# Kernel tuning notes

Hardware: AMD Instinct MI355X
Metric: run time of the kernel (lower is better)

Reference implementation:

```python
import jax, jax.numpy as jnp
import numpy as np

BIT, RW, CW, YR, ID, ZC = 4, 8, 8, 512, 64, 512


def setup_inputs() -> dict:
    key = jax.random.key(0)
    ks = jax.random.split(key, 8)
    return {
        "X": jax.random.normal(ks[0], (4096, CW * ZC), dtype=jnp.float32),
        "Y": jax.random.uniform(ks[1], (BIT, RW, CW, YR, ID), dtype=jnp.float32),
        "Z": jax.random.uniform(ks[2], (BIT, RW, CW, ID, ZC), dtype=jnp.float32),
        "a": jax.random.normal(ks[3], (BIT, RW, CW, 1, 1), dtype=jnp.float32),
        "b": jax.random.normal(ks[4], (BIT, RW, CW, 1, 1), dtype=jnp.float32),
        "c": jax.random.normal(ks[5], (BIT, RW, CW, 1, 1), dtype=jnp.float32),
        "d": jax.random.normal(ks[6], (RW, CW, 1, 1), dtype=jnp.float32),
        "bias": jax.random.normal(ks[7], (RW * YR,), dtype=jnp.float32),
    }


def reference(X, Y, Z, a, b, c, d, bias):
    dtype = X.dtype
    # binary codebook buffers (registered as bool in torch): threshold at 0.5
    Yb = (Y > 0.5).astype(dtype)  # [bit, rw, cw, y_row, inter]
    Zb = (Z > 0.5).astype(dtype)  # [bit, rw, cw, inter, z_col]
    # batched binary matmul: [bit, rw, cw, y_row, z_col]
    W_core = jnp.einsum('brcyi,brciz->brcyz', Yb, Zb)
    Y_sum = jnp.sum(Yb, axis=-1, keepdims=True)  # [bit, rw, cw, y_row, 1]
    Z_sum = jnp.sum(Zb, axis=-2, keepdims=True)  # [bit, rw, cw, 1, z_col]
    W = a * W_core + b * Y_sum + c * Z_sum       # [bit, rw, cw, y_row, z_col]
    W = jnp.sum(W, axis=0) + d                   # [rw, cw, y_row, z_col]
    # permute(0,2,1,3) -> [rw, y_row, cw, z_col] -> [rw*y_row, cw*z_col]
    W = jnp.transpose(W, (0, 2, 1, 3)).reshape(RW * YR, CW * ZC)
    return X @ W.T + bias
```

## Files before the change

kernel.cpp:

```cpp
#include <hip/hip_runtime.h>

#define BITN 4
#define RW 8
#define CW 8
#define YR 512
#define IDIM 64
#define ZC 512
#define NROW 4096
#define KDIM 4096
#define MDIM 4096

#define GAS __attribute__((address_space(1)))
#define LAS __attribute__((address_space(3)))

typedef __attribute__((ext_vector_type(8))) _Float16 f16x8;
typedef __attribute__((ext_vector_type(4))) float f32x4;

__device__ __forceinline__ unsigned short f2h(float v) {
    return __builtin_bit_cast(unsigned short, (_Float16)v);
}

__global__ __launch_bounds__(256) void pack_y_kernel(
    const float* __restrict__ Y, unsigned long long* __restrict__ Ym) {
    const int g = blockIdx.x * 4 + (threadIdx.x >> 6);
    const int lane = threadIdx.x & 63;
    float v = Y[(size_t)g * 64 + lane];
    unsigned long long m = __ballot(v > 0.5f);
    if (lane == 0) Ym[g] = m;
}

__global__ __launch_bounds__(512) void pack_z_kernel(
    const float* __restrict__ Z, unsigned long long* __restrict__ Zm) {
    const int s = blockIdx.x;
    const int z = threadIdx.x;
    const size_t base = (size_t)s * 64 * 512;
    unsigned long long m = 0;
#pragma unroll
    for (int i = 0; i < 64; ++i) {
        float v = Z[base + (size_t)i * 512 + z];
        m |= (unsigned long long)(v > 0.5f) << i;
    }
    Zm[(size_t)s * 512 + z] = m;
}

__global__ __launch_bounds__(512) void build_w_kernel(
    const unsigned long long* __restrict__ Ym, const unsigned long long* __restrict__ Zm,
    const float* __restrict__ Ac, const float* __restrict__ Bc,
    const float* __restrict__ Cc, const float* __restrict__ Dc,
    unsigned short* __restrict__ Wh) {
    const int rc = blockIdx.x;
    const int rw = rc >> 3, cw = rc & 7;
    const int yc = blockIdx.y;
    const int z = threadIdx.x;

    __shared__ unsigned long long sYm[4][128];
    __shared__ float sYt[128];

    unsigned long long zm[4];
    float Ar[4];
    float czd = Dc[rc];
#pragma unroll
    for (int b = 0; b < 4; ++b) {
        zm[b] = Zm[(size_t)(b * 64 + rc) * 512 + z];
        Ar[b] = Ac[b * 64 + rc];
        czd += Cc[b * 64 + rc] * (float)__popcll(zm[b]);
    }
    {
        int b = z >> 7, y = z & 127;
        sYm[b][y] = Ym[(size_t)(b * 64 + rc) * 512 + yc * 128 + y];
    }
    __syncthreads();
    if (z < 128) {
        float t = 0.f;
#pragma unroll
        for (int b = 0; b < 4; ++b)
            t += Bc[b * 64 + rc] * (float)__popcll(sYm[b][z]);
        sYt[z] = t;
    }
    __syncthreads();

    for (int y = 0; y < 128; ++y) {
        float w = sYt[y] + czd;
#pragma unroll
        for (int b = 0; b < 4; ++b)
            w += Ar[b] * (float)__popcll(sYm[b][y] & zm[b]);
        size_t o = (size_t)(rw * 512 + yc * 128 + y) * KDIM + cw * 512 + z;
        Wh[o] = f2h(w);
    }
}

__global__ __launch_bounds__(256) void convert_x_kernel(
    const float* __restrict__ X, unsigned short* __restrict__ Xh) {
    const size_t i = (size_t)blockIdx.x * 256 + threadIdx.x;
    float4 v = reinterpret_cast<const float4*>(X)[i];
    ushort4 h;
    h.x = f2h(v.x);
    h.y = f2h(v.y);
    h.z = f2h(v.z);
    h.w = f2h(v.w);
    reinterpret_cast<ushort4*>(Xh)[i] = h;
}

__global__ __launch_bounds__(256) void gemm_f16_kernel(
    const unsigned short* __restrict__ Xh, const unsigned short* __restrict__ Wh,
    const float* __restrict__ bias, float* __restrict__ out) {
    __shared__ unsigned short sX[128 * 32];
    __shared__ unsigned short sW[128 * 32];

    const int tid = threadIdx.x;
    const int lane = tid & 63;
    const int wave = tid >> 6;
    const int wr = wave >> 1, wc = wave & 1;
    const int fr = lane & 15, fq = lane >> 4;

    const int row0 = blockIdx.y * 128;
    const int col0 = blockIdx.x * 128;

    const int st_row = lane >> 2;
    const int st_k = (lane & 3) * 8;

    f32x4 acc[4][4] = {};

    for (int kt = 0; kt < KDIM; kt += 32) {
        __syncthreads();
#pragma unroll
        for (int r = 0; r < 2; ++r) {
            const int c = r * 4 + wave;
            const int trow = c * 16 + st_row;
            const size_t gA = (size_t)(row0 + trow) * KDIM + kt + st_k;
            const size_t gB = (size_t)(col0 + trow) * KDIM + kt + st_k;
            const int so = c * 512;
            __builtin_amdgcn_global_load_lds((GAS void*)(Xh + gA), (LAS void*)(sX + so), 16, 0, 0);
            __builtin_amdgcn_global_load_lds((GAS void*)(Wh + gB), (LAS void*)(sW + so), 16, 0, 0);
        }
        __syncthreads();

        f16x8 a[4], b[4];
#pragma unroll
        for (int m = 0; m < 4; ++m) {
            const int ro = (64 * wr + 16 * m + fr) * 32 + fq * 8;
            a[m] = *reinterpret_cast<const f16x8*>(&sX[ro]);
        }
#pragma unroll
        for (int n = 0; n < 4; ++n) {
            const int ro = (64 * wc + 16 * n + fr) * 32 + fq * 8;
            b[n] = *reinterpret_cast<const f16x8*>(&sW[ro]);
        }
#pragma unroll
        for (int m = 0; m < 4; ++m)
#pragma unroll
            for (int n = 0; n < 4; ++n)
                acc[m][n] = __builtin_amdgcn_mfma_f32_16x16x32_f16(a[m], b[n], acc[m][n], 0, 0, 0);
    }

    float bvec[4];
#pragma unroll
    for (int n = 0; n < 4; ++n) bvec[n] = bias[col0 + 64 * wc + 16 * n + fr];

#pragma unroll
    for (int m = 0; m < 4; ++m) {
        const int orow = row0 + 64 * wr + 16 * m + 4 * fq;
#pragma unroll
        for (int n = 0; n < 4; ++n) {
            const int ocol = col0 + 64 * wc + 16 * n + fr;
            float* po = out + (size_t)orow * MDIM + ocol;
#pragma unroll
            for (int e = 0; e < 4; ++e)
                po[(size_t)e * MDIM] = acc[m][n][e] + bvec[n];
        }
    }
}

extern "C" void kernel_launch(void* const* d_in, const int* in_sizes, int n_in,
                              void* d_out, int out_size, void* d_ws, size_t ws_size,
                              hipStream_t stream) {
    const float* X  = (const float*)d_in[0];
    const float* Y  = (const float*)d_in[1];
    const float* Z  = (const float*)d_in[2];
    const float* Ac = (const float*)d_in[3];
    const float* Bc = (const float*)d_in[4];
    const float* Cc = (const float*)d_in[5];
    const float* Dc = (const float*)d_in[6];
    const float* bias = (const float*)d_in[7];
    float* out = (float*)d_out;

    char* ws = (char*)d_ws;
    unsigned short* Xh = (unsigned short*)(ws);
    unsigned short* Wh = (unsigned short*)(ws + (size_t)33554432);
    unsigned long long* Ym = (unsigned long long*)(ws + (size_t)67108864);
    unsigned long long* Zm = (unsigned long long*)(ws + (size_t)68157440);

    pack_y_kernel<<<32768, 256, 0, stream>>>(Y, Ym);
    pack_z_kernel<<<256, 512, 0, stream>>>(Z, Zm);
    build_w_kernel<<<dim3(64, 4), 512, 0, stream>>>(Ym, Zm, Ac, Bc, Cc, Dc, Wh);
    convert_x_kernel<<<16384, 256, 0, stream>>>(X, Xh);
    gemm_f16_kernel<<<dim3(32, 32), 256, 0, stream>>>(Xh, Wh, bias, out);
}
```

Baseline: 397.7 us.

## Rewrite GEMM with 256x256 tiles, triple-buffered LDS pipeline, and rework W build

The GEMM moves to 512-thread blocks computing 256x256 tiles, with XOR-swizzled LDS, a three-stage global_load_lds ring buffer, split A/B prefetch interleaved with MFMA phases, s_setprio, and a swizzled block order for L2 locality. The W-build kernel now launches 8x more blocks, has each thread produce four z columns with vectorized ushort4 stores, and drops one barrier. The aim is to hide global load latency behind MFMA work and raise arithmetic intensity per tile, at the cost of heavy register use (128 accumulator floats) and reliance on hand-placed waitcnt counts. The new GEMM grid of 256 blocks fills roughly one wave of CUs.

Result: faster. 333.6 us (-16.1%).

```diff
diff --git a/kernel.cpp b/kernel.cpp
--- a/kernel.cpp
+++ b/kernel.cpp
@@ -1,15 +1,7 @@
 #include <hip/hip_runtime.h>
 
-#define BITN 4
-#define RW 8
-#define CW 8
-#define YR 512
-#define IDIM 64
-#define ZC 512
-#define NROW 4096
 #define KDIM 4096
 #define MDIM 4096
-
 #define GAS __attribute__((address_space(1)))
 #define LAS __attribute__((address_space(3)))
 
@@ -51,41 +43,54 @@
     const int rc = blockIdx.x;
     const int rw = rc >> 3, cw = rc & 7;
     const int yc = blockIdx.y;
-    const int z = threadIdx.x;
-
-    __shared__ unsigned long long sYm[4][128];
-    __shared__ float sYt[128];
-
-    unsigned long long zm[4];
-    float Ar[4];
-    float czd = Dc[rc];
+    const int tid = threadIdx.x;
+    const int zq = tid & 127;
+    const int ys = tid >> 7;
+
+    __shared__ unsigned long long sYm[4][16];
+
+    float Ar[4], Br[4];
+    float dval = Dc[rc];
+    float czd4[4] = {dval, dval, dval, dval};
+    unsigned long long zm[4][4];
 #pragma unroll
     for (int b = 0; b < 4; ++b) {
-        zm[b] = Zm[(size_t)(b * 64 + rc) * 512 + z];
         Ar[b] = Ac[b * 64 + rc];
-        czd += Cc[b * 64 + rc] * (float)__popcll(zm[b]);
-    }
-    {
-        int b = z >> 7, y = z & 127;
-        sYm[b][y] = Ym[(size_t)(b * 64 + rc) * 512 + yc * 128 + y];
-    }
+        Br[b] = Bc[b * 64 + rc];
+        float cb = Cc[b * 64 + rc];
+        const unsigned long long* zp = Zm + (size_t)(b * 64 + rc) * 512 + zq * 4;
+#pragma unroll
+        for (int j = 0; j < 4; ++j) {
+            zm[b][j] = zp[j];
+            czd4[j] += cb * (float)__popcll(zm[b][j]);
+        }
+    }
+    if (tid < 64)
+        sYm[tid >> 4][tid & 15] = Ym[(size_t)((tid >> 4) * 64 + rc) * 512 + yc * 16 + (tid & 15)];
     __syncthreads();
-    if (z < 128) {
-        float t = 0.f;
-#pragma unroll
-        for (int b = 0; b < 4; ++b)
-            t += Bc[b * 64 + rc] * (float)__popcll(sYm[b][z]);
-        sYt[z] = t;
-    }
-    __syncthreads();
-
-    for (int y = 0; y < 128; ++y) {
-        float w = sYt[y] + czd;
-#pragma unroll
-        for (int b = 0; b < 4; ++b)
-            w += Ar[b] * (float)__popcll(sYm[b][y] & zm[b]);
-        size_t o = (size_t)(rw * 512 + yc * 128 + y) * KDIM + cw * 512 + z;
-        Wh[o] = f2h(w);
+
+#pragma unroll
+    for (int yy = 0; yy < 4; ++yy) {
+        const int yl = ys * 4 + yy;
+        unsigned long long ym[4];
+        float bt = 0.f;
+#pragma unroll
+        for (int b = 0; b < 4; ++b) {
+            ym[b] = sYm[b][yl];
+            bt += Br[b] * (float)__popcll(ym[b]);
+        }
+        ushort4 o4;
+        float w0 = bt + czd4[0], w1 = bt + czd4[1], w2 = bt + czd4[2], w3 = bt + czd4[3];
+#pragma unroll
+        for (int b = 0; b < 4; ++b) {
+            w0 += Ar[b] * (float)__popcll(ym[b] & zm[b][0]);
+            w1 += Ar[b] * (float)__popcll(ym[b] & zm[b][1]);
+            w2 += Ar[b] * (float)__popcll(ym[b] & zm[b][2]);
+            w3 += Ar[b] * (float)__popcll(ym[b] & zm[b][3]);
+        }
+        o4.x = f2h(w0); o4.y = f2h(w1); o4.z = f2h(w2); o4.w = f2h(w3);
+        size_t o = (size_t)(rw * 512 + yc * 16 + yl) * KDIM + cw * 512 + zq * 4;
+        *reinterpret_cast<ushort4*>(&Wh[o]) = o4;
     }
 }
 
@@ -94,79 +99,125 @@
     const size_t i = (size_t)blockIdx.x * 256 + threadIdx.x;
     float4 v = reinterpret_cast<const float4*>(X)[i];
     ushort4 h;
-    h.x = f2h(v.x);
-    h.y = f2h(v.y);
-    h.z = f2h(v.z);
-    h.w = f2h(v.w);
+    h.x = f2h(v.x); h.y = f2h(v.y); h.z = f2h(v.z); h.w = f2h(v.w);
     reinterpret_cast<ushort4*>(Xh)[i] = h;
 }
 
-__global__ __launch_bounds__(256) void gemm_f16_kernel(
+__global__ __launch_bounds__(512) void gemm_f16_kernel(
     const unsigned short* __restrict__ Xh, const unsigned short* __restrict__ Wh,
     const float* __restrict__ bias, float* __restrict__ out) {
-    __shared__ unsigned short sX[128 * 32];
-    __shared__ unsigned short sW[128 * 32];
+    __shared__ unsigned short smem[49152];
 
     const int tid = threadIdx.x;
     const int lane = tid & 63;
     const int wave = tid >> 6;
-    const int wr = wave >> 1, wc = wave & 1;
+    const int wr = wave >> 2, wc = wave & 3;
     const int fr = lane & 15, fq = lane >> 4;
 
-    const int row0 = blockIdx.y * 128;
-    const int col0 = blockIdx.x * 128;
-
-    const int st_row = lane >> 2;
-    const int st_k = (lane & 3) * 8;
-
-    f32x4 acc[4][4] = {};
-
-    for (int kt = 0; kt < KDIM; kt += 32) {
-        __syncthreads();
-#pragma unroll
-        for (int r = 0; r < 2; ++r) {
-            const int c = r * 4 + wave;
-            const int trow = c * 16 + st_row;
-            const size_t gA = (size_t)(row0 + trow) * KDIM + kt + st_k;
-            const size_t gB = (size_t)(col0 + trow) * KDIM + kt + st_k;
-            const int so = c * 512;
-            __builtin_amdgcn_global_load_lds((GAS void*)(Xh + gA), (LAS void*)(sX + so), 16, 0, 0);
-            __builtin_amdgcn_global_load_lds((GAS void*)(Wh + gB), (LAS void*)(sW + so), 16, 0, 0);
-        }
-        __syncthreads();
-
-        f16x8 a[4], b[4];
-#pragma unroll
-        for (int m = 0; m < 4; ++m) {
-            const int ro = (64 * wr + 16 * m + fr) * 32 + fq * 8;
-            a[m] = *reinterpret_cast<const f16x8*>(&sX[ro]);
-        }
+    const int bid = blockIdx.x;
+    const int swz = (bid & 7) * 32 + (bid >> 3);
+    const int bx = swz & 15, by = swz >> 4;
+    const int row0 = by * 256, col0 = bx * 256;
+
+    int goff[2];
+#pragma unroll
+    for (int uh = 0; uh < 2; ++uh) {
+        int d = uh * 8192 + tid * 16;
+        int e = d ^ (((d >> 7) & 7) << 4);
+        int rowl = ((e >> 7) << 1) | ((e >> 6) & 1);
+        int kel = (e >> 1) & 31;
+        goff[uh] = rowl * KDIM + kel;
+    }
+
+    const int sw = (fr >> 1) << 3;
+    int idxA[8], idxB[4];
+#pragma unroll
+    for (int m = 0; m < 8; ++m)
+        idxA[m] = ((wr * 64 + m * 8 + (fr >> 1)) * 64 + (fr & 1) * 32 + fq * 8) ^ sw;
+#pragma unroll
+    for (int n = 0; n < 4; ++n)
+        idxB[n] = ((wc * 32 + n * 8 + (fr >> 1)) * 64 + (fr & 1) * 32 + fq * 8) ^ sw;
+
+    const unsigned short* Abase = Xh + (size_t)row0 * KDIM;
+    const unsigned short* Bbase = Wh + (size_t)col0 * KDIM;
+    const int ldsw = wave * 512;
+
+    f32x4 acc[8][4] = {};
+
+#pragma unroll
+    for (int t = 0; t < 2; ++t) {
+        const int ub = t * 16384;
+#pragma unroll
+        for (int uh = 0; uh < 2; ++uh) {
+            __builtin_amdgcn_global_load_lds((GAS void*)(Abase + t * 32 + goff[uh]),
+                (LAS void*)(smem + ub + uh * 4096 + ldsw), 16, 0, 0);
+            __builtin_amdgcn_global_load_lds((GAS void*)(Bbase + t * 32 + goff[uh]),
+                (LAS void*)(smem + ub + 8192 + uh * 4096 + ldsw), 16, 0, 0);
+        }
+    }
+    asm volatile("s_waitcnt vmcnt(4)" ::: "memory");
+    __builtin_amdgcn_s_barrier();
+
+    int cb = 0;
+    for (int t = 0; t < 128; ++t) {
+        const int nb = (cb >= 16384) ? cb - 16384 : cb + 32768;
+        const int tk = (t < 126) ? (t + 2) * 32 : 0;
+
+        f16x8 a0[4], bfr[4];
+#pragma unroll
+        for (int m = 0; m < 4; ++m) a0[m] = *reinterpret_cast<const f16x8*>(&smem[cb + idxA[m]]);
+#pragma unroll
+        for (int n = 0; n < 4; ++n) bfr[n] = *reinterpret_cast<const f16x8*>(&smem[cb + 8192 + idxB[n]]);
+#pragma unroll
+        for (int uh = 0; uh < 2; ++uh)
+            __builtin_amdgcn_global_load_lds((GAS void*)(Abase + tk + goff[uh]),
+                (LAS void*)(smem + nb + uh * 4096 + ldsw), 16, 0, 0);
+        __builtin_amdgcn_s_barrier();
+        __builtin_amdgcn_s_setprio(1);
+#pragma unroll
+        for (int m = 0; m < 4; ++m)
+#pragma unroll
+            for (int n = 0; n < 4; ++n)
+                acc[m][n] = __builtin_amdgcn_mfma_f32_16x16x32_f16(a0[m], bfr[n], acc[m][n], 0, 0, 0);
+        __builtin_amdgcn_s_setprio(0);
+        __builtin_amdgcn_s_barrier();
+
+        f16x8 a1[4];
+#pragma unroll
+        for (int m = 0; m < 4; ++m) a1[m] = *reinterpret_cast<const f16x8*>(&smem[cb + idxA[4 + m]]);
+#pragma unroll
+        for (int uh = 0; uh < 2; ++uh)
+            __builtin_amdgcn_global_load_lds((GAS void*)(Bbase + tk + goff[uh]),
+                (LAS void*)(smem + nb + 8192 + uh * 4096 + ldsw), 16, 0, 0);
+        __builtin_amdgcn_s_barrier();
+        __builtin_amdgcn_s_setprio(1);
+#pragma unroll
+        for (int m = 0; m < 4; ++m)
+#pragma unroll
+            for (int n = 0; n < 4; ++n)
+                acc[4 + m][n] = __builtin_amdgcn_mfma_f32_16x16x32_f16(a1[m], bfr[n], acc[4 + m][n], 0, 0, 0);
+        __builtin_amdgcn_s_setprio(0);
+        asm volatile("s_waitcnt vmcnt(4)" ::: "memory");
+        __builtin_amdgcn_s_barrier();
+
+        cb = (cb == 32768) ? 0 : cb + 16384;
+    }
+    asm volatile("s_waitcnt vmcnt(0)" ::: "memory");
+
+    float bv[4];
+#pragma unroll
+    for (int n = 0; n < 4; ++n) bv[n] = bias[col0 + wc * 64 + n * 16 + fr];
+
+#pragma unroll
+    for (int m = 0; m < 8; ++m) {
+        const int orow = row0 + wr * 128 + m * 16 + fq * 4;
 #pragma unroll
         for (int n = 0; n < 4; ++n) {
-            const int ro = (64 * wc + 16 * n + fr) * 32 + fq * 8;
-            b[n] = *reinterpret_cast<const f16x8*>(&sW[ro]);
-        }
-#pragma unroll
-        for (int m = 0; m < 4; ++m)
-#pragma unroll
-            for (int n = 0; n < 4; ++n)
-                acc[m][n] = __builtin_amdgcn_mfma_f32_16x16x32_f16(a[m], b[n], acc[m][n], 0, 0, 0);
-    }
-
-    float bvec[4];
-#pragma unroll
-    for (int n = 0; n < 4; ++n) bvec[n] = bias[col0 + 64 * wc + 16 * n + fr];
-
-#pragma unroll
-    for (int m = 0; m < 4; ++m) {
-        const int orow = row0 + 64 * wr + 16 * m + 4 * fq;
-#pragma unroll
-        for (int n = 0; n < 4; ++n) {
-            const int ocol = col0 + 64 * wc + 16 * n + fr;
+            const int ocol = col0 + wc * 64 + n * 16 + fr;
             float* po = out + (size_t)orow * MDIM + ocol;
 #pragma unroll
             for (int e = 0; e < 4; ++e)
-                po[(size_t)e * MDIM] = acc[m][n][e] + bvec[n];
+                po[(size_t)e * MDIM] = acc[m][n][e] + bv[n];
         }
     }
 }
@@ -192,7 +243,7 @@
 
     pack_y_kernel<<<32768, 256, 0, stream>>>(Y, Ym);
     pack_z_kernel<<<256, 512, 0, stream>>>(Z, Zm);
-    build_w_kernel<<<dim3(64, 4), 512, 0, stream>>>(Ym, Zm, Ac, Bc, Cc, Dc, Wh);
+    build_w_kernel<<<dim3(64, 32), 512, 0, stream>>>(Ym, Zm, Ac, Bc, Cc, Dc, Wh);
     convert_x_kernel<<<16384, 256, 0, stream>>>(X, Xh);
-    gemm_f16_kernel<<<dim3(32, 32), 256, 0, stream>>>(Xh, Wh, bias, out);
-}
+    gemm_f16_kernel<<<dim3(256), 512, 0, stream>>>(Xh, Wh, bias, out);
+}
```
